# Performance work log

Measured on AMD Instinct MI355X. Metric: run time of the kernel, lower is better.

## Reference

```python
import jax, jax.numpy as jnp
import numpy as np


def setup_inputs() -> dict:
    key = jax.random.key(0)
    k1, k2 = jax.random.split(key)
    return {
        "embeddings": jax.random.normal(k1, (4, 768, 32, 32), dtype=jnp.float32),
        "database": jax.random.normal(k2, (20000, 768), dtype=jnp.float32),
        "k": 3,
        "out_h": 512,
        "out_w": 512,
    }


def reference(embeddings, database, k, out_h, out_w):
    # embeddings: [B, D, h, w]  (segmenter hidden state), database: [N, D]
    B, D, h, w = embeddings.shape
    # B x h x w x D -> B x (h*w) x D query layout, as in _get_ood_scores
    q = jnp.transpose(embeddings, (0, 2, 3, 1)).reshape(B, h * w, D)
    # squared Euclidean distances via (||q||^2 + ||x||^2 - 2 q.x)
    q2 = jnp.sum(q * q, axis=-1)[..., None]                 # [B, hw, 1]
    x2 = jnp.sum(database * database, axis=-1)[None, None]  # [1, 1, N]
    d2 = q2 + x2 - 2.0 * jnp.einsum("bqd,nd->bqn", q, database)
    dist = jnp.sqrt(jnp.maximum(d2, 1e-12))                 # [B, hw, N]
    # k smallest distances (sklearn kneighbors) then mean over neighbors
    neg_topk, _ = jax.lax.top_k(-dist, k)                   # [B, hw, k]
    ood = jnp.mean(-neg_topk, axis=-1).reshape(B, h, w)
    # F.interpolate(..., mode='bilinear', align_corners=False) == half-pixel bilinear
    ood_up = jax.image.resize(ood[:, None], (B, 1, out_h, out_w), method="bilinear")
    return ood_up
```

## Files before the change

kernel.cpp:

```cpp
#include <hip/hip_runtime.h>
#include <hip/hip_bf16.h>
#include <math.h>

constexpr int B    = 4;
constexpr int D    = 768;
constexpr int HW   = 1024;
constexpr int M    = B * HW;
constexpr int NDB  = 20000;
constexpr int LT   = 158;
constexpr int NDBP = LT * 128;
constexpr int OUTH = 512;
constexpr int OUTW = 512;

constexpr int BM     = 256;
constexpr int BN     = 128;
constexpr int KSTEPS = D / 64;
constexpr int NSPLIT = 16;
constexpr int NT2    = 79;
constexpr int STEPB  = 128 * 64;

typedef int   i32x8  __attribute__((ext_vector_type(8)));
typedef float f32x16 __attribute__((ext_vector_type(16)));

__device__ __forceinline__ void insert3(float& t0, float& t1, float& t2, float d) {
    float a0 = fminf(d, t0);
    float b0 = fmaxf(d, t0);
    float a1 = fminf(b0, t1);
    float b1 = fmaxf(b0, t1);
    t0 = a0; t1 = a1;
    t2 = fminf(b1, t2);
}

__device__ __forceinline__ unsigned int pack4_fp8(float a, float b, float c, float d) {
    int v = __builtin_amdgcn_cvt_pk_fp8_f32(a, b, 0, false);
    v = __builtin_amdgcn_cvt_pk_fp8_f32(c, d, v, true);
    return (unsigned int)v;
}

__device__ __forceinline__ void gl_lds16(const unsigned char* g, unsigned char* l) {
    __builtin_amdgcn_global_load_lds(
        (const __attribute__((address_space(1))) void*)g,
        (__attribute__((address_space(3))) void*)l, 16, 0, 0);
}

__global__ __launch_bounds__(256) void db_convert(const float* __restrict__ db,
                                                  uint4* __restrict__ dbt8,
                                                  float* __restrict__ x2p) {
    __shared__ float panel[128][68];
    __shared__ float part[512];
    const int lt = blockIdx.x;
    const int g  = blockIdx.y;
    const int t  = threadIdx.x;
    const int n0 = lt * 128;

    #pragma unroll
    for (int pass = 0; pass < 8; ++pass) {
        int idx = pass * 256 + t;
        int row = idx >> 4, c4 = idx & 15;
        int n = n0 + row;
        float4 v = make_float4(0.f, 0.f, 0.f, 0.f);
        if (n < NDB) v = *(const float4*)(db + (size_t)n * D + g * 64 + c4 * 4);
        *(float4*)&panel[row][c4 * 4] = v;
    }
    __syncthreads();
    #pragma unroll
    for (int pass = 0; pass < 2; ++pass) {
        int idx = pass * 256 + t;
        int r  = idx & 31;
        int kc = (idx >> 5) & 1;
        int h2 = (idx >> 6) & 1;
        int rg = idx >> 7;
        int row  = rg * 32 + r;
        int kloc = kc * 32 + h2 * 16;
        float4 va = *(const float4*)&panel[row][kloc + 0];
        float4 vb = *(const float4*)&panel[row][kloc + 4];
        float4 vc = *(const float4*)&panel[row][kloc + 8];
        float4 vd = *(const float4*)&panel[row][kloc + 12];
        float ss = va.x*va.x + va.y*va.y + va.z*va.z + va.w*va.w
                 + vb.x*vb.x + vb.y*vb.y + vb.z*vb.z + vb.w*vb.w
                 + vc.x*vc.x + vc.y*vc.y + vc.z*vc.z + vc.w*vc.w
                 + vd.x*vd.x + vd.y*vd.y + vd.z*vd.z + vd.w*vd.w;
        uint4 o;
        o.x = pack4_fp8(va.x, va.y, va.z, va.w);
        o.y = pack4_fp8(vb.x, vb.y, vb.z, vb.w);
        o.z = pack4_fp8(vc.x, vc.y, vc.z, vc.w);
        o.w = pack4_fp8(vd.x, vd.y, vd.z, vd.w);
        dbt8[((size_t)lt * KSTEPS + g) * 512 + idx] = o;
        part[idx] = ss;
    }
    __syncthreads();
    if (t < 128) {
        int base = (t >> 5) * 128 + (t & 31);
        float s = part[base] + part[base + 32] + part[base + 64] + part[base + 96];
        x2p[((size_t)lt * KSTEPS + g) * 128 + t] = s;
    }
}

__global__ __launch_bounds__(256) void q_convert(const float* __restrict__ emb,
                                                 uint4* __restrict__ qbt8,
                                                 float* __restrict__ q2p) {
    __shared__ float part[512];
    const int qt = blockIdx.x;
    const int g  = blockIdx.y;
    const int t  = threadIdx.x;
    const int b  = qt >> 3;
    const int p0 = (qt & 7) * 128;

    #pragma unroll
    for (int pass = 0; pass < 2; ++pass) {
        int idx = pass * 256 + t;
        int r  = idx & 31;
        int kc = (idx >> 5) & 1;
        int h2 = (idx >> 6) & 1;
        int rg = idx >> 7;
        int prow = rg * 32 + r;
        int kb = g * 64 + kc * 32 + h2 * 16;
        const float* src = emb + ((size_t)b * D + kb) * HW + p0 + prow;
        float v[16];
        float ss = 0.f;
        #pragma unroll
        for (int j = 0; j < 16; ++j) {
            v[j] = src[(size_t)j * HW];
            ss = fmaf(v[j], v[j], ss);
        }
        uint4 o;
        o.x = pack4_fp8(-2.f*v[0],  -2.f*v[1],  -2.f*v[2],  -2.f*v[3]);
        o.y = pack4_fp8(-2.f*v[4],  -2.f*v[5],  -2.f*v[6],  -2.f*v[7]);
        o.z = pack4_fp8(-2.f*v[8],  -2.f*v[9],  -2.f*v[10], -2.f*v[11]);
        o.w = pack4_fp8(-2.f*v[12], -2.f*v[13], -2.f*v[14], -2.f*v[15]);
        qbt8[((size_t)qt * KSTEPS + g) * 512 + idx] = o;
        part[idx] = ss;
    }
    __syncthreads();
    if (t < 128) {
        int base = (t >> 5) * 128 + (t & 31);
        float s = part[base] + part[base + 32] + part[base + 64] + part[base + 96];
        q2p[((size_t)qt * KSTEPS + g) * 128 + t] = s;
    }
}

__global__ __launch_bounds__(256, 2) void gemm_topk(const unsigned char* __restrict__ dbt8,
                                                    const unsigned char* __restrict__ qbt8,
                                                    const float* __restrict__ x2p,
                                                    float* __restrict__ partials) {
    __shared__ __align__(16) unsigned char Asm[2 * 16384];
    __shared__ __align__(16) unsigned char Bsm[2 * 8192];
    __shared__ float X2s[BM];
    __shared__ float red[4][BN][3];

    const int tid  = threadIdx.x;
    const int lane = tid & 63;
    const int w    = tid >> 6;
    const int lts  = w >> 1;
    const int wr   = w & 1;
    const int h    = lane >> 5;
    const int l31  = lane & 31;

    const int bid   = blockIdx.x;
    const int xcd   = bid & 7;
    const int j     = bid >> 3;
    const int sp    = xcd + 8 * (j >> 5);
    const int qtile = j & 31;
    const int m0    = qtile * BN;

    int a_off[2], b_off[4];
    #pragma unroll
    for (int i = 0; i < 2; ++i) a_off[i] = lts * 8192 + (wr * 2 + i) * 2048 + h * 512 + l31 * 16;
    #pragma unroll
    for (int j4 = 0; j4 < 4; ++j4) b_off[j4] = j4 * 2048 + h * 512 + l31 * 16;

    const unsigned char* aNext = dbt8 + (size_t)(2 * sp + lts) * KSTEPS * STEPB + wr * 4096 + lane * 16;
    const unsigned char* bNext = qbt8 + (size_t)qtile * KSTEPS * STEPB + w * 2048 + lane * 16;
    unsigned char* aDst = Asm + w * 4096;
    unsigned char* bDst = Bsm + w * 2048;

    #pragma unroll
    for (int l = 0; l < 4; ++l) gl_lds16(aNext + l * 1024, aDst + l * 1024);
    #pragma unroll
    for (int l = 0; l < 2; ++l) gl_lds16(bNext + l * 1024, bDst + l * 1024);

    float t0[4], t1[4], t2[4];
    #pragma unroll
    for (int j4 = 0; j4 < 4; ++j4) { t0[j4] = INFINITY; t1[j4] = INFINITY; t2[j4] = INFINITY; }

    for (int tile = sp; tile < NT2; tile += NSPLIT) {
        __syncthreads();
        {
            int n = tile * BM + tid;
            float s = 1e30f;
            if (n < NDB) {
                const float* p = x2p + (size_t)(n >> 7) * (KSTEPS * 128) + (n & 127);
                s = 0.f;
                #pragma unroll
                for (int g = 0; g < KSTEPS; ++g) s += p[g * 128];
            }
            X2s[tid] = s;
        }

        f32x16 acc[2][4];
        #pragma unroll
        for (int i = 0; i < 2; ++i)
            #pragma unroll
            for (int j4 = 0; j4 < 4; ++j4)
                #pragma unroll
                for (int r = 0; r < 16; ++r) acc[i][j4][r] = 0.f;

        const bool lastTile = (tile + NSPLIT >= NT2);

        #pragma unroll 2
        for (int g = 0; g < KSTEPS; ++g) {
            const int cur = g & 1;
            __syncthreads();
            if (g < KSTEPS - 1) {
                aNext += STEPB;
                bNext += STEPB;
                unsigned char* ad = aDst + (cur ^ 1) * 16384;
                unsigned char* bd = bDst + (cur ^ 1) * 8192;
                #pragma unroll
                for (int l = 0; l < 4; ++l) gl_lds16(aNext + l * 1024, ad + l * 1024);
                #pragma unroll
                for (int l = 0; l < 2; ++l) gl_lds16(bNext + l * 1024, bd + l * 1024);
            } else if (!lastTile) {
                aNext += (size_t)(2 * NSPLIT) * KSTEPS * STEPB - (KSTEPS - 1) * STEPB;
                bNext -= (size_t)(KSTEPS - 1) * STEPB;
                unsigned char* ad = aDst + (cur ^ 1) * 16384;
                unsigned char* bd = bDst + (cur ^ 1) * 8192;
                #pragma unroll
                for (int l = 0; l < 4; ++l) gl_lds16(aNext + l * 1024, ad + l * 1024);
                #pragma unroll
                for (int l = 0; l < 2; ++l) gl_lds16(bNext + l * 1024, bd + l * 1024);
            }
            const unsigned char* Ab = Asm + cur * 16384;
            const unsigned char* Bb = Bsm + cur * 8192;
            i32x8 af[2], bf[4];
            #pragma unroll
            for (int i = 0; i < 2; ++i) {
                int4 lo = *(const int4*)(Ab + a_off[i]);
                int4 hi = *(const int4*)(Ab + a_off[i] + 1024);
                af[i] = (i32x8){lo.x, lo.y, lo.z, lo.w, hi.x, hi.y, hi.z, hi.w};
            }
            #pragma unroll
            for (int j4 = 0; j4 < 4; ++j4) {
                int4 lo = *(const int4*)(Bb + b_off[j4]);
                int4 hi = *(const int4*)(Bb + b_off[j4] + 1024);
                bf[j4] = (i32x8){lo.x, lo.y, lo.z, lo.w, hi.x, hi.y, hi.z, hi.w};
            }
            #pragma unroll
            for (int i = 0; i < 2; ++i)
                #pragma unroll
                for (int j4 = 0; j4 < 4; ++j4)
                    acc[i][j4] = __builtin_amdgcn_mfma_scale_f32_32x32x64_f8f6f4(
                        af[i], bf[j4], acc[i][j4], 0, 0,
                        0, 0x7f7f7f7f, 0, 0x7f7f7f7f);
        }

        #pragma unroll
        for (int i = 0; i < 2; ++i) {
            #pragma unroll
            for (int rg2 = 0; rg2 < 4; ++rg2) {
                float4 xv = *(const float4*)&X2s[w * 64 + i * 32 + rg2 * 8 + 4 * h];
                #pragma unroll
                for (int j4 = 0; j4 < 4; ++j4) {
                    #pragma unroll
                    for (int rr = 0; rr < 4; ++rr) {
                        float s = acc[i][j4][rg2 * 4 + rr] + ((const float*)&xv)[rr];
                        insert3(t0[j4], t1[j4], t2[j4], s);
                    }
                }
            }
        }
    }

    #pragma unroll
    for (int j4 = 0; j4 < 4; ++j4) {
        float o0 = __shfl_xor(t0[j4], 32);
        float o1 = __shfl_xor(t1[j4], 32);
        float o2 = __shfl_xor(t2[j4], 32);
        insert3(t0[j4], t1[j4], t2[j4], o0);
        insert3(t0[j4], t1[j4], t2[j4], o1);
        insert3(t0[j4], t1[j4], t2[j4], o2);
    }
    if (h == 0) {
        #pragma unroll
        for (int j4 = 0; j4 < 4; ++j4) {
            int col = j4 * 32 + l31;
            red[w][col][0] = t0[j4];
            red[w][col][1] = t1[j4];
            red[w][col][2] = t2[j4];
        }
    }
    __syncthreads();
    if (tid < BN) {
        float a0 = red[0][tid][0], a1 = red[0][tid][1], a2 = red[0][tid][2];
        #pragma unroll
        for (int ww = 1; ww < 4; ++ww) {
            insert3(a0, a1, a2, red[ww][tid][0]);
            insert3(a0, a1, a2, red[ww][tid][1]);
            insert3(a0, a1, a2, red[ww][tid][2]);
        }
        float* dst = partials + ((size_t)(m0 + tid) * NSPLIT + sp) * 3;
        dst[0] = a0; dst[1] = a1; dst[2] = a2;
    }
}

__global__ __launch_bounds__(256) void merge_ood(const float* __restrict__ partials,
                                                 const float* __restrict__ q2p,
                                                 float* __restrict__ ood) {
    int m = blockIdx.x * 256 + threadIdx.x;
    if (m >= M) return;
    const float* pp = partials + (size_t)m * NSPLIT * 3;
    float a0 = INFINITY, a1 = INFINITY, a2 = INFINITY;
    #pragma unroll
    for (int j = 0; j < NSPLIT * 3; ++j) insert3(a0, a1, a2, pp[j]);
    const float* qp = q2p + (size_t)(m >> 7) * KSTEPS * 128 + (m & 127);
    float q = 0.f;
    #pragma unroll
    for (int g = 0; g < KSTEPS; ++g) q += qp[g * 128];
    float d0 = sqrtf(fmaxf(q + a0, 1e-12f));
    float d1 = sqrtf(fmaxf(q + a1, 1e-12f));
    float d2 = sqrtf(fmaxf(q + a2, 1e-12f));
    ood[m] = (d0 + d1 + d2) * (1.f / 3.f);
}

__global__ __launch_bounds__(256) void upsample(const float* __restrict__ ood,
                                                float* __restrict__ out) {
    int idx = blockIdx.x * 256 + threadIdx.x;
    int ox = idx & (OUTW - 1);
    int oy = (idx >> 9) & (OUTH - 1);
    int bb = idx >> 18;
    float sx = (ox + 0.5f) * (32.f / OUTW) - 0.5f;
    float sy = (oy + 0.5f) * (32.f / OUTH) - 0.5f;
    float fx = floorf(sx), fy = floorf(sy);
    float wx = sx - fx, wy = sy - fy;
    int x0 = max(0, min(31, (int)fx));
    int x1 = max(0, min(31, (int)fx + 1));
    int y0 = max(0, min(31, (int)fy));
    int y1 = max(0, min(31, (int)fy + 1));
    const float* src = ood + bb * 1024;
    float v00 = src[y0 * 32 + x0];
    float v01 = src[y0 * 32 + x1];
    float v10 = src[y1 * 32 + x0];
    float v11 = src[y1 * 32 + x1];
    float top = v00 + wx * (v01 - v00);
    float bot = v10 + wx * (v11 - v10);
    out[idx] = top + wy * (bot - top);
}

extern "C" void kernel_launch(void* const* d_in, const int* in_sizes, int n_in,
                              void* d_out, int out_size, void* d_ws, size_t ws_size,
                              hipStream_t stream) {
    const float* emb = (const float*)d_in[0];
    const float* db  = (const float*)d_in[1];
    float* out = (float*)d_out;

    char* ws = (char*)d_ws;
    unsigned char* dbt8 = (unsigned char*)ws;
    unsigned char* qbt8 = (unsigned char*)(ws + 15532032);
    float* x2p      = (float*)(ws + 18677760);
    float* q2p      = (float*)(ws + 19648512);
    float* ood      = (float*)(ws + 19845120);
    float* partials = (float*)(ws + 19861504);

    db_convert<<<dim3(LT, KSTEPS), 256, 0, stream>>>(db, (uint4*)dbt8, x2p);
    q_convert<<<dim3(32, KSTEPS), 256, 0, stream>>>(emb, (uint4*)qbt8, q2p);
    gemm_topk<<<NSPLIT * 32, 256, 0, stream>>>(dbt8, qbt8, x2p, partials);
    merge_ood<<<(M + 255) / 256, 256, 0, stream>>>(partials, q2p, ood);
    upsample<<<(B * OUTH * OUTW) / 256, 256, 0, stream>>>(ood, out);
}
```

Measured before the change: 186.4 us.

## Triple-buffer LDS and software-pipeline fragment reads ahead of MFMA

```diff
diff --git a/kernel.cpp b/kernel.cpp
--- a/kernel.cpp
+++ b/kernel.cpp
@@ -18,6 +18,9 @@
 constexpr int NSPLIT = 16;
 constexpr int NT2    = 79;
 constexpr int STEPB  = 128 * 64;
+
+constexpr int ABUF = 16384;
+constexpr int BBUF = 8192;
 
 typedef int   i32x8  __attribute__((ext_vector_type(8)));
 typedef float f32x16 __attribute__((ext_vector_type(16)));
@@ -143,8 +146,8 @@
                                                     const unsigned char* __restrict__ qbt8,
                                                     const float* __restrict__ x2p,
                                                     float* __restrict__ partials) {
-    __shared__ __align__(16) unsigned char Asm[2 * 16384];
-    __shared__ __align__(16) unsigned char Bsm[2 * 8192];
+    __shared__ __align__(16) unsigned char Asm[3 * ABUF];
+    __shared__ __align__(16) unsigned char Bsm[3 * BBUF];
     __shared__ float X2s[BM];
     __shared__ float red[4][BN][3];
 
@@ -169,91 +172,51 @@
     #pragma unroll
     for (int j4 = 0; j4 < 4; ++j4) b_off[j4] = j4 * 2048 + h * 512 + l31 * 16;
 
-    const unsigned char* aNext = dbt8 + (size_t)(2 * sp + lts) * KSTEPS * STEPB + wr * 4096 + lane * 16;
-    const unsigned char* bNext = qbt8 + (size_t)qtile * KSTEPS * STEPB + w * 2048 + lane * 16;
-    unsigned char* aDst = Asm + w * 4096;
-    unsigned char* bDst = Bsm + w * 2048;
-
-    #pragma unroll
-    for (int l = 0; l < 4; ++l) gl_lds16(aNext + l * 1024, aDst + l * 1024);
-    #pragma unroll
-    for (int l = 0; l < 2; ++l) gl_lds16(bNext + l * 1024, bDst + l * 1024);
+    const unsigned char* aC = dbt8 + (size_t)(2 * sp + lts) * KSTEPS * STEPB + wr * 4096 + lane * 16;
+    const unsigned char* bC = qbt8 + (size_t)qtile * KSTEPS * STEPB + w * 2048 + lane * 16;
+    int gs = 0;
+
+    auto advance = [&]() {
+        if (gs == KSTEPS - 1) {
+            aC += (size_t)(2 * NSPLIT) * KSTEPS * STEPB - (size_t)(KSTEPS - 1) * STEPB;
+            bC -= (size_t)(KSTEPS - 1) * STEPB;
+            gs = 0;
+        } else {
+            aC += STEPB; bC += STEPB; ++gs;
+        }
+    };
+    auto stage_to = [&](int bi) {
+        unsigned char* ad = Asm + bi * ABUF + w * 4096;
+        unsigned char* bd = Bsm + bi * BBUF + w * 2048;
+        #pragma unroll
+        for (int l = 0; l < 4; ++l) gl_lds16(aC + l * 1024, ad + l * 1024);
+        #pragma unroll
+        for (int l = 0; l < 2; ++l) gl_lds16(bC + l * 1024, bd + l * 1024);
+    };
+    auto read_frags = [&](int bi, i32x8 (&af)[2], i32x8 (&bf)[4]) {
+        const unsigned char* Ab = Asm + bi * ABUF;
+        const unsigned char* Bb = Bsm + bi * BBUF;
+        #pragma unroll
+        for (int i = 0; i < 2; ++i) {
+            int4 lo = *(const int4*)(Ab + a_off[i]);
+            int4 hi = *(const int4*)(Ab + a_off[i] + 1024);
+            af[i] = (i32x8){lo.x, lo.y, lo.z, lo.w, hi.x, hi.y, hi.z, hi.w};
+        }
+        #pragma unroll
+        for (int j4 = 0; j4 < 4; ++j4) {
+            int4 lo = *(const int4*)(Bb + b_off[j4]);
+            int4 hi = *(const int4*)(Bb + b_off[j4] + 1024);
+            bf[j4] = (i32x8){lo.x, lo.y, lo.z, lo.w, hi.x, hi.y, hi.z, hi.w};
+        }
+    };
 
     float t0[4], t1[4], t2[4];
     #pragma unroll
     for (int j4 = 0; j4 < 4; ++j4) { t0[j4] = INFINITY; t1[j4] = INFINITY; t2[j4] = INFINITY; }
 
-    for (int tile = sp; tile < NT2; tile += NSPLIT) {
-        __syncthreads();
-        {
-            int n = tile * BM + tid;
-            float s = 1e30f;
-            if (n < NDB) {
-                const float* p = x2p + (size_t)(n >> 7) * (KSTEPS * 128) + (n & 127);
-                s = 0.f;
-                #pragma unroll
-                for (int g = 0; g < KSTEPS; ++g) s += p[g * 128];
-            }
-            X2s[tid] = s;
-        }
-
-        f32x16 acc[2][4];
-        #pragma unroll
-        for (int i = 0; i < 2; ++i)
-            #pragma unroll
-            for (int j4 = 0; j4 < 4; ++j4)
-                #pragma unroll
-                for (int r = 0; r < 16; ++r) acc[i][j4][r] = 0.f;
-
-        const bool lastTile = (tile + NSPLIT >= NT2);
-
-        #pragma unroll 2
-        for (int g = 0; g < KSTEPS; ++g) {
-            const int cur = g & 1;
-            __syncthreads();
-            if (g < KSTEPS - 1) {
-                aNext += STEPB;
-                bNext += STEPB;
-                unsigned char* ad = aDst + (cur ^ 1) * 16384;
-                unsigned char* bd = bDst + (cur ^ 1) * 8192;
-                #pragma unroll
-                for (int l = 0; l < 4; ++l) gl_lds16(aNext + l * 1024, ad + l * 1024);
-                #pragma unroll
-                for (int l = 0; l < 2; ++l) gl_lds16(bNext + l * 1024, bd + l * 1024);
-            } else if (!lastTile) {
-                aNext += (size_t)(2 * NSPLIT) * KSTEPS * STEPB - (KSTEPS - 1) * STEPB;
-                bNext -= (size_t)(KSTEPS - 1) * STEPB;
-                unsigned char* ad = aDst + (cur ^ 1) * 16384;
-                unsigned char* bd = bDst + (cur ^ 1) * 8192;
-                #pragma unroll
-                for (int l = 0; l < 4; ++l) gl_lds16(aNext + l * 1024, ad + l * 1024);
-                #pragma unroll
-                for (int l = 0; l < 2; ++l) gl_lds16(bNext + l * 1024, bd + l * 1024);
-            }
-            const unsigned char* Ab = Asm + cur * 16384;
-            const unsigned char* Bb = Bsm + cur * 8192;
-            i32x8 af[2], bf[4];
-            #pragma unroll
-            for (int i = 0; i < 2; ++i) {
-                int4 lo = *(const int4*)(Ab + a_off[i]);
-                int4 hi = *(const int4*)(Ab + a_off[i] + 1024);
-                af[i] = (i32x8){lo.x, lo.y, lo.z, lo.w, hi.x, hi.y, hi.z, hi.w};
-            }
-            #pragma unroll
-            for (int j4 = 0; j4 < 4; ++j4) {
-                int4 lo = *(const int4*)(Bb + b_off[j4]);
-                int4 hi = *(const int4*)(Bb + b_off[j4] + 1024);
-                bf[j4] = (i32x8){lo.x, lo.y, lo.z, lo.w, hi.x, hi.y, hi.z, hi.w};
-            }
-            #pragma unroll
-            for (int i = 0; i < 2; ++i)
-                #pragma unroll
-                for (int j4 = 0; j4 < 4; ++j4)
-                    acc[i][j4] = __builtin_amdgcn_mfma_scale_f32_32x32x64_f8f6f4(
-                        af[i], bf[j4], acc[i][j4], 0, 0,
-                        0, 0x7f7f7f7f, 0, 0x7f7f7f7f);
-        }
-
+    f32x16 acc[2][4];
+
+    auto epilogue = [&]() {
         #pragma unroll
         for (int i = 0; i < 2; ++i) {
             #pragma unroll
@@ -263,13 +226,94 @@
                 for (int j4 = 0; j4 < 4; ++j4) {
                     #pragma unroll
                     for (int rr = 0; rr < 4; ++rr) {
-                        float s = acc[i][j4][rg2 * 4 + rr] + ((const float*)&xv)[rr];
-                        insert3(t0[j4], t1[j4], t2[j4], s);
+                        float sv = acc[i][j4][rg2 * 4 + rr] + ((const float*)&xv)[rr];
+                        insert3(t0[j4], t1[j4], t2[j4], sv);
                     }
                 }
             }
         }
-    }
+    };
+    auto do_mfma = [&](const i32x8 (&af)[2], const i32x8 (&bf)[4]) {
+        __builtin_amdgcn_s_setprio(1);
+        #pragma unroll
+        for (int i = 0; i < 2; ++i)
+            #pragma unroll
+            for (int j4 = 0; j4 < 4; ++j4)
+                acc[i][j4] = __builtin_amdgcn_mfma_scale_f32_32x32x64_f8f6f4(
+                    af[i], bf[j4], acc[i][j4], 0, 0,
+                    0, 0x7f7f7f7f, 0, 0x7f7f7f7f);
+        __builtin_amdgcn_s_setprio(0);
+    };
+
+    int ntiles = 0;
+    for (int t = sp; t < NT2; t += NSPLIT) ++ntiles;
+    const int S = ntiles * KSTEPS;
+
+    stage_to(0); advance();
+    stage_to(1); advance();
+    asm volatile("s_waitcnt vmcnt(6)" ::: "memory");
+    __builtin_amdgcn_s_barrier();
+    i32x8 afA[2], bfA[4], afB[2], bfB[4];
+    read_frags(0, afA, bfA);
+
+    int br = 1;
+    int bs = 2;
+    int tile = sp;
+
+    for (int s = 0; s < S; s += 2) {
+        if ((s % KSTEPS) == 0) {
+            if (s) epilogue();
+            __syncthreads();
+            {
+                int n = tile * BM + tid;
+                float xs = 1e30f;
+                if (n < NDB) {
+                    const float* p = x2p + (size_t)(n >> 7) * (KSTEPS * 128) + (n & 127);
+                    xs = 0.f;
+                    #pragma unroll
+                    for (int g = 0; g < KSTEPS; ++g) xs += p[g * 128];
+                }
+                X2s[tid] = xs;
+            }
+            tile += NSPLIT;
+            #pragma unroll
+            for (int i = 0; i < 2; ++i)
+                #pragma unroll
+                for (int j4 = 0; j4 < 4; ++j4)
+                    #pragma unroll
+                    for (int r = 0; r < 16; ++r) acc[i][j4][r] = 0.f;
+        }
+        if (s + 2 < S) {
+            stage_to(bs); advance();
+            asm volatile("s_waitcnt vmcnt(6)" ::: "memory");
+        } else {
+            asm volatile("s_waitcnt vmcnt(0)" ::: "memory");
+        }
+        asm volatile("s_waitcnt lgkmcnt(0)" ::: "memory");
+        __builtin_amdgcn_sched_barrier(0);
+        __builtin_amdgcn_s_barrier();
+        read_frags(br, afB, bfB);
+        __builtin_amdgcn_sched_barrier(0);
+        do_mfma(afA, bfA);
+        bs = (bs == 2) ? 0 : bs + 1;
+        br = (br == 2) ? 0 : br + 1;
+
+        if (s + 3 < S) {
+            stage_to(bs); advance();
+            asm volatile("s_waitcnt vmcnt(6)" ::: "memory");
+        } else {
+            asm volatile("s_waitcnt vmcnt(0)" ::: "memory");
+        }
+        asm volatile("s_waitcnt lgkmcnt(0)" ::: "memory");
+        __builtin_amdgcn_sched_barrier(0);
+        __builtin_amdgcn_s_barrier();
+        if (s + 2 < S) read_frags(br, afA, bfA);
+        __builtin_amdgcn_sched_barrier(0);
+        do_mfma(afB, bfB);
+        bs = (bs == 2) ? 0 : bs + 1;
+        br = (br == 2) ? 0 : br + 1;
+    }
+    epilogue();
 
     #pragma unroll
     for (int j4 = 0; j4 < 4; ++j4) {
```

After: 184.6 us. About the same (-1.0%).

## Keep query tile resident in LDS and stream database fragments directly to registers

Applied to the files above, without the earlier changes.

```diff
diff --git a/kernel.cpp b/kernel.cpp
--- a/kernel.cpp
+++ b/kernel.cpp
@@ -7,16 +7,15 @@
 constexpr int HW   = 1024;
 constexpr int M    = B * HW;
 constexpr int NDB  = 20000;
-constexpr int LT   = 158;
-constexpr int NDBP = LT * 128;
+constexpr int LTP  = 160;
 constexpr int OUTH = 512;
 constexpr int OUTW = 512;
 
-constexpr int BM     = 256;
+constexpr int BM     = 512;
 constexpr int BN     = 128;
 constexpr int KSTEPS = D / 64;
-constexpr int NSPLIT = 16;
-constexpr int NT2    = 79;
+constexpr int NSPLIT = 8;
+constexpr int NT     = 40;
 constexpr int STEPB  = 128 * 64;
 
 typedef int   i32x8  __attribute__((ext_vector_type(8)));
@@ -139,62 +138,64 @@
     }
 }
 
-__global__ __launch_bounds__(256, 2) void gemm_topk(const unsigned char* __restrict__ dbt8,
+__global__ __launch_bounds__(512, 2) void gemm_topk(const unsigned char* __restrict__ dbt8,
                                                     const unsigned char* __restrict__ qbt8,
                                                     const float* __restrict__ x2p,
                                                     float* __restrict__ partials) {
-    __shared__ __align__(16) unsigned char Asm[2 * 16384];
-    __shared__ __align__(16) unsigned char Bsm[2 * 8192];
-    __shared__ float X2s[BM];
-    __shared__ float red[4][BN][3];
+    __shared__ __align__(16) unsigned char Bq[KSTEPS * 8192];
+    __shared__ float red[8][BN][3];
 
     const int tid  = threadIdx.x;
     const int lane = tid & 63;
     const int w    = tid >> 6;
-    const int lts  = w >> 1;
-    const int wr   = w & 1;
     const int h    = lane >> 5;
     const int l31  = lane & 31;
 
     const int bid   = blockIdx.x;
-    const int xcd   = bid & 7;
-    const int j     = bid >> 3;
-    const int sp    = xcd + 8 * (j >> 5);
-    const int qtile = j & 31;
+    const int sp    = bid & 7;
+    const int qtile = bid >> 3;
     const int m0    = qtile * BN;
 
-    int a_off[2], b_off[4];
-    #pragma unroll
-    for (int i = 0; i < 2; ++i) a_off[i] = lts * 8192 + (wr * 2 + i) * 2048 + h * 512 + l31 * 16;
+    {
+        const unsigned char* qb = qbt8 + (size_t)qtile * KSTEPS * STEPB;
+        #pragma unroll
+        for (int p = 0; p < 12; ++p) {
+            int idx = p * 512 + tid;
+            gl_lds16(qb + (size_t)idx * 16, Bq + idx * 16);
+        }
+    }
+    __syncthreads();
+
+    int b_off[4];
     #pragma unroll
     for (int j4 = 0; j4 < 4; ++j4) b_off[j4] = j4 * 2048 + h * 512 + l31 * 16;
 
-    const unsigned char* aNext = dbt8 + (size_t)(2 * sp + lts) * KSTEPS * STEPB + wr * 4096 + lane * 16;
-    const unsigned char* bNext = qbt8 + (size_t)qtile * KSTEPS * STEPB + w * 2048 + lane * 16;
-    unsigned char* aDst = Asm + w * 4096;
-    unsigned char* bDst = Bsm + w * 2048;
-
-    #pragma unroll
-    for (int l = 0; l < 4; ++l) gl_lds16(aNext + l * 1024, aDst + l * 1024);
-    #pragma unroll
-    for (int l = 0; l < 2; ++l) gl_lds16(bNext + l * 1024, bDst + l * 1024);
-
     float t0[4], t1[4], t2[4];
     #pragma unroll
     for (int j4 = 0; j4 < 4; ++j4) { t0[j4] = INFINITY; t1[j4] = INFINITY; t2[j4] = INFINITY; }
 
-    for (int tile = sp; tile < NT2; tile += NSPLIT) {
-        __syncthreads();
+    const unsigned char* aP = dbt8 + ((size_t)(4 * sp + (w >> 1)) * KSTEPS) * STEPB
+                              + (w & 1) * 4096 + h * 512 + l31 * 16;
+
+    auto ldA = [&](i32x8& x0, i32x8& x1, const unsigned char* p) {
+        int4 a = *(const int4*)(p);
+        int4 b = *(const int4*)(p + 1024);
+        int4 c = *(const int4*)(p + 2048);
+        int4 d = *(const int4*)(p + 3072);
+        x0 = (i32x8){a.x, a.y, a.z, a.w, b.x, b.y, b.z, b.w};
+        x1 = (i32x8){c.x, c.y, c.z, c.w, d.x, d.y, d.z, d.w};
+    };
+
+    for (int t = sp; t < NT; t += NSPLIT) {
+        float sx = 1e30f;
         {
-            int n = tile * BM + tid;
-            float s = 1e30f;
+            int n = t * 512 + w * 64 + lane;
             if (n < NDB) {
                 const float* p = x2p + (size_t)(n >> 7) * (KSTEPS * 128) + (n & 127);
-                s = 0.f;
+                sx = 0.f;
                 #pragma unroll
-                for (int g = 0; g < KSTEPS; ++g) s += p[g * 128];
+                for (int g = 0; g < KSTEPS; ++g) sx += p[g * 128];
             }
-            X2s[tid] = s;
         }
 
         f32x16 acc[2][4];
@@ -205,67 +206,43 @@
                 #pragma unroll
                 for (int r = 0; r < 16; ++r) acc[i][j4][r] = 0.f;
 
-        const bool lastTile = (tile + NSPLIT >= NT2);
-
-        #pragma unroll 2
+        i32x8 af0, af1, an0, an1;
+        const unsigned char* aPtr = aP;
+        ldA(af0, af1, aPtr); aPtr += STEPB;
+        #pragma unroll
         for (int g = 0; g < KSTEPS; ++g) {
-            const int cur = g & 1;
-            __syncthreads();
-            if (g < KSTEPS - 1) {
-                aNext += STEPB;
-                bNext += STEPB;
-                unsigned char* ad = aDst + (cur ^ 1) * 16384;
-                unsigned char* bd = bDst + (cur ^ 1) * 8192;
-                #pragma unroll
-                for (int l = 0; l < 4; ++l) gl_lds16(aNext + l * 1024, ad + l * 1024);
-                #pragma unroll
-                for (int l = 0; l < 2; ++l) gl_lds16(bNext + l * 1024, bd + l * 1024);
-            } else if (!lastTile) {
-                aNext += (size_t)(2 * NSPLIT) * KSTEPS * STEPB - (KSTEPS - 1) * STEPB;
-                bNext -= (size_t)(KSTEPS - 1) * STEPB;
-                unsigned char* ad = aDst + (cur ^ 1) * 16384;
-                unsigned char* bd = bDst + (cur ^ 1) * 8192;
-                #pragma unroll
-                for (int l = 0; l < 4; ++l) gl_lds16(aNext + l * 1024, ad + l * 1024);
-                #pragma unroll
-                for (int l = 0; l < 2; ++l) gl_lds16(bNext + l * 1024, bd + l * 1024);
-            }
-            const unsigned char* Ab = Asm + cur * 16384;
-            const unsigned char* Bb = Bsm + cur * 8192;
-            i32x8 af[2], bf[4];
-            #pragma unroll
-            for (int i = 0; i < 2; ++i) {
-                int4 lo = *(const int4*)(Ab + a_off[i]);
-                int4 hi = *(const int4*)(Ab + a_off[i] + 1024);
-                af[i] = (i32x8){lo.x, lo.y, lo.z, lo.w, hi.x, hi.y, hi.z, hi.w};
-            }
+            if (g + 1 < KSTEPS) { ldA(an0, an1, aPtr); aPtr += STEPB; }
+            const unsigned char* Bb = Bq + g * 8192;
+            i32x8 bf[4];
             #pragma unroll
             for (int j4 = 0; j4 < 4; ++j4) {
                 int4 lo = *(const int4*)(Bb + b_off[j4]);
                 int4 hi = *(const int4*)(Bb + b_off[j4] + 1024);
                 bf[j4] = (i32x8){lo.x, lo.y, lo.z, lo.w, hi.x, hi.y, hi.z, hi.w};
             }
+            __builtin_amdgcn_s_setprio(1);
             #pragma unroll
-            for (int i = 0; i < 2; ++i)
-                #pragma unroll
-                for (int j4 = 0; j4 < 4; ++j4)
-                    acc[i][j4] = __builtin_amdgcn_mfma_scale_f32_32x32x64_f8f6f4(
-                        af[i], bf[j4], acc[i][j4], 0, 0,
-                        0, 0x7f7f7f7f, 0, 0x7f7f7f7f);
-        }
+            for (int j4 = 0; j4 < 4; ++j4) {
+                acc[0][j4] = __builtin_amdgcn_mfma_scale_f32_32x32x64_f8f6f4(
+                    af0, bf[j4], acc[0][j4], 0, 0, 0, 0x7f7f7f7f, 0, 0x7f7f7f7f);
+                acc[1][j4] = __builtin_amdgcn_mfma_scale_f32_32x32x64_f8f6f4(
+                    af1, bf[j4], acc[1][j4], 0, 0, 0, 0x7f7f7f7f, 0, 0x7f7f7f7f);
+            }
+            __builtin_amdgcn_s_setprio(0);
+            af0 = an0; af1 = an1;
+        }
+        aP += (size_t)32 * KSTEPS * STEPB;
 
         #pragma unroll
         for (int i = 0; i < 2; ++i) {
             #pragma unroll
             for (int rg2 = 0; rg2 < 4; ++rg2) {
-                float4 xv = *(const float4*)&X2s[w * 64 + i * 32 + rg2 * 8 + 4 * h];
                 #pragma unroll
-                for (int j4 = 0; j4 < 4; ++j4) {
+                for (int rr = 0; rr < 4; ++rr) {
+                    float xv = __shfl(sx, i * 32 + rg2 * 8 + 4 * h + rr);
                     #pragma unroll
-                    for (int rr = 0; rr < 4; ++rr) {
-                        float s = acc[i][j4][rg2 * 4 + rr] + ((const float*)&xv)[rr];
-                        insert3(t0[j4], t1[j4], t2[j4], s);
-                    }
+                    for (int j4 = 0; j4 < 4; ++j4)
+                        insert3(t0[j4], t1[j4], t2[j4], acc[i][j4][rg2 * 4 + rr] + xv);
                 }
             }
         }
@@ -293,7 +270,7 @@
     if (tid < BN) {
         float a0 = red[0][tid][0], a1 = red[0][tid][1], a2 = red[0][tid][2];
         #pragma unroll
-        for (int ww = 1; ww < 4; ++ww) {
+        for (int ww = 1; ww < 8; ++ww) {
             insert3(a0, a1, a2, red[ww][tid][0]);
             insert3(a0, a1, a2, red[ww][tid][1]);
             insert3(a0, a1, a2, red[ww][tid][2]);
@@ -355,15 +332,15 @@
 
     char* ws = (char*)d_ws;
     unsigned char* dbt8 = (unsigned char*)ws;
-    unsigned char* qbt8 = (unsigned char*)(ws + 15532032);
-    float* x2p      = (float*)(ws + 18677760);
-    float* q2p      = (float*)(ws + 19648512);
-    float* ood      = (float*)(ws + 19845120);
-    float* partials = (float*)(ws + 19861504);
-
-    db_convert<<<dim3(LT, KSTEPS), 256, 0, stream>>>(db, (uint4*)dbt8, x2p);
+    unsigned char* qbt8 = (unsigned char*)(ws + 15728640);
+    float* x2p      = (float*)(ws + 18874368);
+    float* q2p      = (float*)(ws + 19857408);
+    float* ood      = (float*)(ws + 20054016);
+    float* partials = (float*)(ws + 20070400);
+
+    db_convert<<<dim3(LTP, KSTEPS), 256, 0, stream>>>(db, (uint4*)dbt8, x2p);
     q_convert<<<dim3(32, KSTEPS), 256, 0, stream>>>(emb, (uint4*)qbt8, q2p);
-    gemm_topk<<<NSPLIT * 32, 256, 0, stream>>>(dbt8, qbt8, x2p, partials);
+    gemm_topk<<<NSPLIT * 32, 512, 0, stream>>>(dbt8, qbt8, x2p, partials);
     merge_ood<<<(M + 255) / 256, 256, 0, stream>>>(partials, q2p, ood);
     upsample<<<(B * OUTH * OUTW) / 256, 256, 0, stream>>>(ood, out);
 }
```

Result: slower. 219.8 us (+17.9%).
